# Kernel tuning notes

Measured on AMD Instinct MI355X. Metric: run time of the kernel, lower is better.

## Reference

```python
import jax, jax.numpy as jnp
import numpy as np

B, CI, CO, H, W = 16, 256, 256, 64, 64
WDIM, NUM_FREQ, FREQ_DIM = 512, 16, 512
KS, PAD = 3, 1
SR = 64.0
LR_MULT = 1.0 / SR
GAIN = float(np.sqrt(1.0 / (CI * KS * KS)))
FREQ_GAIN = float(np.sqrt(1.0 / (FREQ_DIM * 2)))


def setup_inputs() -> dict:
    key = jax.random.key(0)
    ks = jax.random.split(key, 7)
    x = jax.random.normal(ks[0], (B, CI, H, W), dtype=jnp.float32)
    temb = jax.random.normal(ks[1], (B, WDIM), dtype=jnp.float32)
    basis = jax.random.normal(ks[2], (CI, KS, KS, FREQ_DIM), dtype=jnp.float32)
    magnitude = jax.random.normal(ks[3], (NUM_FREQ, CI, FREQ_DIM), dtype=jnp.float32)
    out_linear = jax.random.normal(ks[4], (CO, FREQ_DIM), dtype=jnp.float32)
    # FullyConnectedLayer init: weight = randn * (weight_init/lr_mult) = randn (both 1/SR)
    affine_w = jax.random.normal(ks[5], (NUM_FREQ, WDIM), dtype=jnp.float32)
    # bias param stores bias_init / lr_mult = 1 / (1/SR) = SR
    affine_b = jnp.full((NUM_FREQ,), SR, dtype=jnp.float32)
    conv_bias = jnp.zeros((CO,), dtype=jnp.float32)
    return {"x": x, "temb": temb, "basis": basis, "magnitude": magnitude,
            "out_linear": out_linear, "affine_w": affine_w, "affine_b": affine_b,
            "conv_bias": conv_bias}


def reference(x, temb, basis, magnitude, out_linear, affine_w, affine_b, conv_bias):
    # affine (FullyConnectedLayer, linear activation)
    w = affine_w * (LR_MULT / np.sqrt(WDIM))          # weight_gain
    s = temb @ w.T + affine_b * LR_MULT               # [B, K] per-sample freq weights
    # mix magnitude per sample: [K,I,F],[B,K] -> [B,I,F]
    mag_b = jnp.einsum('kif,bk->bif', magnitude, s) / np.sqrt(NUM_FREQ)
    # per-sample dynamic kernels: [I,h,w,F],[B,I,F],[O,F] -> [B,O,I,h,w]
    kernel = jnp.einsum('ihwf,bif,of->boihw', basis, mag_b, out_linear)
    kernel = kernel * (FREQ_GAIN * GAIN)
    kernel = kernel.reshape(B * CO, CI, KS, KS)
    # grouped conv, groups = batch
    xg = x.reshape(1, B * CI, H, W)
    y = jax.lax.conv_general_dilated(
        xg, kernel, window_strides=(1, 1), padding=[(PAD, PAD), (PAD, PAD)],
        dimension_numbers=('NCHW', 'OIHW', 'NCHW'), feature_group_count=B)
    y = y.reshape(B, CO, H, W)
    return jax.nn.silu(y) + conv_bias[None, :, None, None]
```

## Files before the change

kernel.cpp:

```cpp
#include <hip/hip_runtime.h>
#include <hip/hip_bf16.h>
#include <math.h>

#define B_    16
#define CI_   256
#define CO_   256
#define H_    64
#define W_    64
#define WDIM_ 512
#define NF_   16
#define FD_   512

typedef short bf16x8 __attribute__((ext_vector_type(8)));
typedef short s16x8  __attribute__((ext_vector_type(8)));
typedef float f32x4  __attribute__((ext_vector_type(4)));

__device__ __forceinline__ short f2bf(float f) {
  union { float f; unsigned u; } x; x.f = f;
  unsigned r = (x.u + 0x7FFFu + ((x.u >> 16) & 1u)) >> 16;
  return (short)r;
}
__device__ __forceinline__ float bf2f(short s) {
  union { unsigned u; float f; } x; x.u = ((unsigned)(unsigned short)s) << 16;
  return x.f;
}

__device__ __forceinline__ void gload16(const short* g, short* l) {
  __builtin_amdgcn_global_load_lds(
      (const __attribute__((address_space(1))) void*)g,
      (__attribute__((address_space(3))) void*)l, 16, 0, 0);
}

__device__ __forceinline__ size_t koff(int b, int kb, int cc, int t, int o) {
  return ((((((size_t)b * 4 + kb) * 8 + cc) * 9 + t) * 256) + o) * 8;
}
__device__ __forceinline__ size_t xoff(int b, int kb, int cc, int hp, int wp) {
  return ((((((size_t)b * 4 + kb) * 8 + cc) * 66 + hp) * 66) + wp) * 8;
}

__global__ __launch_bounds__(256) void prep_kernel(
    const float* __restrict__ temb, const float* __restrict__ affine_w,
    const float* __restrict__ affine_b, const float* __restrict__ out_linear,
    float* __restrict__ s_ws, short* __restrict__ olbf) {
  int tid = threadIdx.x;
  if (blockIdx.x == 0) {
    int b = tid >> 4, k = tid & 15;
    const float* t = temb + b * WDIM_;
    const float* w = affine_w + k * WDIM_;
    float acc = 0.f;
    for (int j = 0; j < WDIM_; j += 4) {
      float4 tv = *(const float4*)(t + j);
      float4 wv = *(const float4*)(w + j);
      acc += tv.x * wv.x + tv.y * wv.y + tv.z * wv.z + tv.w * wv.w;
    }
    const float WGAIN = 6.9053399e-4f;
    const float LRM   = 1.0f / 64.0f;
    s_ws[tid] = acc * WGAIN + affine_b[k] * LRM;
  } else {
    int e = (blockIdx.x - 1) * 256 + tid;
    const float* src = out_linear + (size_t)e * 8;
    s16x8 pk;
#pragma unroll
    for (int j = 0; j < 8; ++j) pk[j] = f2bf(src[j]);
    *(s16x8*)(olbf + (size_t)e * 8) = pk;
  }
}

__global__ __launch_bounds__(256) void magmix_kernel(
    const float* __restrict__ magnitude, const float* __restrict__ s_ws,
    short* __restrict__ mag_bf) {
  int bid = blockIdx.x;
  int i = bid >> 1;
  int f = ((bid & 1) << 8) + threadIdx.x;
  __shared__ float ssh[256];
  ssh[threadIdx.x] = s_ws[threadIdx.x];
  __syncthreads();
  float mg[16];
#pragma unroll
  for (int k = 0; k < 16; ++k)
    mg[k] = magnitude[(size_t)(k * CI_ + i) * FD_ + f];
#pragma unroll
  for (int b = 0; b < 16; ++b) {
    float acc = 0.f;
#pragma unroll
    for (int k = 0; k < 16; ++k) acc += mg[k] * ssh[b * 16 + k];
    mag_bf[(size_t)(b * CI_ + i) * FD_ + f] = f2bf(acc * 0.25f);
  }
}

__global__ __launch_bounds__(512) void kernsynth_mfma_kernel(
    const float* __restrict__ basis, const short* __restrict__ mag_bf,
    const short* __restrict__ olbf, short* __restrict__ kbf) {
  int bid = blockIdx.x;
  int b  = bid / 18;
  int mt = bid - b * 18;
  int t   = mt >> 1;
  int i0g = (mt & 1) * 128;

  int tid = threadIdx.x;
  int lane = tid & 63;
  int wv = tid >> 6;
  int wm = wv >> 2, wn = wv & 3;
  int l15 = lane & 15, kb = lane >> 4;

  __shared__ short alds[128 * 64];
  __shared__ short blds[256 * 64];

  f32x4 acc[4][4];
#pragma unroll
  for (int m = 0; m < 4; ++m)
#pragma unroll
    for (int n = 0; n < 4; ++n) acc[m][n] = (f32x4)0.f;

  int ra = tid >> 2;
  int fsa = (tid & 3) * 16;
  int rb = tid >> 1;
  int fsb = (tid & 1) * 32;

  const float* bpA = basis + ((size_t)(i0g + ra) * 9 + t) * FD_ + fsa;
  const short* mpA = mag_bf + ((size_t)b * CI_ + i0g + ra) * FD_ + fsa;
  const short* opB = olbf + (size_t)rb * FD_ + fsb;

  for (int cc = 0; cc < 8; ++cc) {
    int f0 = cc * 64;
    __syncthreads();
#pragma unroll
    for (int u = 0; u < 2; ++u) {
      s16x8 m8 = *(const s16x8*)(mpA + f0 + u * 8);
      s16x8 pk;
#pragma unroll
      for (int j = 0; j < 2; ++j) {
        float4 b4 = *(const float4*)(bpA + f0 + u * 8 + j * 4);
        pk[j * 4 + 0] = f2bf(b4.x * bf2f(m8[j * 4 + 0]));
        pk[j * 4 + 1] = f2bf(b4.y * bf2f(m8[j * 4 + 1]));
        pk[j * 4 + 2] = f2bf(b4.z * bf2f(m8[j * 4 + 2]));
        pk[j * 4 + 3] = f2bf(b4.w * bf2f(m8[j * 4 + 3]));
      }
      int slot = (tid & 3) * 2 + u;
      *(s16x8*)&alds[ra * 64 + ((slot ^ (ra & 7)) << 3)] = pk;
    }
#pragma unroll
    for (int u = 0; u < 4; ++u) {
      s16x8 pk = *(const s16x8*)(opB + f0 + u * 8);
      int slot = (tid & 1) * 4 + u;
      *(s16x8*)&blds[rb * 64 + ((slot ^ (rb & 7)) << 3)] = pk;
    }
    __syncthreads();

#pragma unroll
    for (int ks = 0; ks < 2; ++ks) {
      bf16x8 afr[4], bfr[4];
#pragma unroll
      for (int m = 0; m < 4; ++m) {
        int row = wm * 64 + m * 16 + l15;
        int slot = ks * 4 + kb;
        afr[m] = *(const bf16x8*)&alds[row * 64 + ((slot ^ (row & 7)) << 3)];
      }
#pragma unroll
      for (int n = 0; n < 4; ++n) {
        int row = wn * 64 + n * 16 + l15;
        int slot = ks * 4 + kb;
        bfr[n] = *(const bf16x8*)&blds[row * 64 + ((slot ^ (row & 7)) << 3)];
      }
#pragma unroll
      for (int m = 0; m < 4; ++m)
#pragma unroll
        for (int n = 0; n < 4; ++n)
          acc[m][n] = __builtin_amdgcn_mfma_f32_16x16x32_bf16(afr[m], bfr[n], acc[m][n], 0, 0, 0);
    }
  }

  const float KSCALE = 1.0f / 1536.0f;
#pragma unroll
  for (int m = 0; m < 4; ++m) {
    int i_loc = i0g + wm * 64 + m * 16 + (lane >> 4) * 4;
    int kb2 = (i_loc >> 3) & 3;
    int cc2 = i_loc >> 5;
    int e2  = i_loc & 7;
#pragma unroll
    for (int n = 0; n < 4; ++n) {
      int o = wn * 64 + n * 16 + l15;
      short4 s4;
      s4.x = f2bf(acc[m][n][0] * KSCALE);
      s4.y = f2bf(acc[m][n][1] * KSCALE);
      s4.z = f2bf(acc[m][n][2] * KSCALE);
      s4.w = f2bf(acc[m][n][3] * KSCALE);
      *(short4*)(kbf + koff(b, kb2, cc2, t, o) + e2) = s4;
    }
  }
}

__global__ __launch_bounds__(256) void xpose_kernel(
    const float* __restrict__ x, short* __restrict__ xt) {
  int bid = blockIdx.x;
  int b = bid / 66, hp = bid - b * 66;
  int tid = threadIdx.x;
  s16x8 z = (s16x8)0;
  if (hp == 0 || hp == 65) {
    for (int e = tid; e < 32 * 66; e += 256) {
      int s = e / 66, w = e - s * 66;
      *(s16x8*)(xt + xoff(b, s >> 3, s & 7, hp, w)) = z;
    }
    return;
  }
  int h = hp - 1;
  if (tid < 64) {
    int s = tid >> 1, wslot = (tid & 1) ? 65 : 0;
    *(s16x8*)(xt + xoff(b, s >> 3, s & 7, hp, wslot)) = z;
  }
  __shared__ float lx[32 * 64];
  const float* xb = x + ((size_t)b * CI_) * H_ * W_ + (size_t)h * W_;
  int w = tid >> 2, kb = tid & 3;
  for (int cc = 0; cc < 8; ++cc) {
    __syncthreads();
    {
      int rr = tid >> 4, c4 = (tid & 15) * 4;
      float4 v0 = *(const float4*)(xb + (size_t)(cc * 32 + rr) * H_ * W_ + c4);
      *(float4*)&lx[rr * 64 + c4] = v0;
      float4 v1 = *(const float4*)(xb + (size_t)(cc * 32 + rr + 16) * H_ * W_ + c4);
      *(float4*)&lx[(rr + 16) * 64 + c4] = v1;
    }
    __syncthreads();
    s16x8 o8;
#pragma unroll
    for (int k2 = 0; k2 < 8; ++k2) o8[k2] = f2bf(lx[(kb * 8 + k2) * 64 + w]);
    *(s16x8*)(xt + xoff(b, kb, cc, hp, w + 1)) = o8;
  }
}

__global__ __launch_bounds__(256, 4) void conv_mfma_kernel(
    const short* __restrict__ xt, const short* __restrict__ kbf,
    const float* __restrict__ conv_bias, float* __restrict__ out) {
  int bid = ((blockIdx.x & 7) << 7) + (blockIdx.x >> 3);
  int b  = bid >> 6;
  int ot = (bid >> 4) & 3;
  int rt = bid & 15;
  int o_base = ot * 64;
  int r0 = rt * 4;
  int tid = threadIdx.x;
  int lane = tid & 63;
  int wv = tid >> 6;
  int orow = lane & 15, kb = lane >> 4;

  __shared__ short xs[25 * 512];

  f32x4 acc[4][4];
#pragma unroll
  for (int m = 0; m < 4; ++m)
#pragma unroll
    for (int n = 0; n < 4; ++n) acc[m][n] = (f32x4)0.f;

  const short* abase = kbf + koff(b, kb, 0, 0, o_base + orow);

  for (int cc = 0; cc < 8; ++cc) {
    __syncthreads();
    for (int ch = wv; ch < 25; ch += 4) {
      int D = ch * 1024 + lane * 16;
      int kb2 = D / 6400;
      int r = (D - kb2 * 6400) >> 4;
      r = r < 396 ? r : 395;
      int xr = (r * 1986) >> 17;
      int c = r - xr * 66;
      const short* src = xt + xoff(b, kb2, cc, r0 + xr, c);
      gload16(src, &xs[ch * 512]);
    }
    __syncthreads();

    const short* ac = abase + (size_t)cc * 18432;
#pragma unroll
    for (int t = 0; t < 9; ++t) {
      const int dh = t / 3 - 1, dw = t % 3 - 1;
      bf16x8 afr[4], bfr[4];
#pragma unroll
      for (int m = 0; m < 4; ++m)
        afr[m] = *(const bf16x8*)(ac + t * 2048 + m * 128);
      int xr = wv + 1 + dh;
#pragma unroll
      for (int n = 0; n < 4; ++n) {
        int xc = n * 16 + orow + 1 + dw;
        bfr[n] = *(const bf16x8*)&xs[(kb * 400 + xr * 66 + xc) * 8];
      }
#pragma unroll
      for (int m = 0; m < 4; ++m)
#pragma unroll
        for (int n = 0; n < 4; ++n)
          acc[m][n] = __builtin_amdgcn_mfma_f32_16x16x32_bf16(afr[m], bfr[n], acc[m][n], 0, 0, 0);
    }
  }

  int row = r0 + wv;
#pragma unroll
  for (int m = 0; m < 4; ++m) {
#pragma unroll
    for (int q = 0; q < 4; ++q) {
      int o = o_base + m * 16 + (lane >> 4) * 4 + q;
      float bias = conv_bias[o];
      size_t obase = (((size_t)b * CO_ + o) * H_ + row) * W_;
#pragma unroll
      for (int n = 0; n < 4; ++n) {
        float y = acc[m][n][q];
        out[obase + n * 16 + (lane & 15)] = y / (1.f + __expf(-y)) + bias;
      }
    }
  }
}

extern "C" void kernel_launch(void* const* d_in, const int* in_sizes, int n_in,
                              void* d_out, int out_size, void* d_ws, size_t ws_size,
                              hipStream_t stream) {
  const float* x          = (const float*)d_in[0];
  const float* temb       = (const float*)d_in[1];
  const float* basis      = (const float*)d_in[2];
  const float* magnitude  = (const float*)d_in[3];
  const float* out_linear = (const float*)d_in[4];
  const float* affine_w   = (const float*)d_in[5];
  const float* affine_b   = (const float*)d_in[6];
  const float* conv_bias  = (const float*)d_in[7];
  float* out = (float*)d_out;

  char* ws = (char*)d_ws;
  float* s_ws = (float*)ws;
  short* kbf  = (short*)(ws + 1024);
  short* xt   = (short*)(ws + 1024 + 18874368);
  short* mag_bf = (short*)(ws + 1024 + 18874368);
  short* olbf   = (short*)(ws + 1024 + 18874368 + 4194304);

  prep_kernel<<<65, 256, 0, stream>>>(temb, affine_w, affine_b, out_linear, s_ws, olbf);
  magmix_kernel<<<512, 256, 0, stream>>>(magnitude, s_ws, mag_bf);
  kernsynth_mfma_kernel<<<288, 512, 0, stream>>>(basis, mag_bf, olbf, kbf);
  xpose_kernel<<<16 * 66, 256, 0, stream>>>(x, xt);
  conv_mfma_kernel<<<1024, 256, 0, stream>>>(xt, kbf, conv_bias, out);
}
```

Before: 150.1 us.

## Merge kernel synthesis and input transpose into one heterogeneous launch

```diff
diff --git a/kernel.cpp b/kernel.cpp
--- a/kernel.cpp
+++ b/kernel.cpp
@@ -88,143 +88,149 @@
   }
 }
 
-__global__ __launch_bounds__(512) void kernsynth_mfma_kernel(
+__global__ __launch_bounds__(512) void synth_xpose_kernel(
     const float* __restrict__ basis, const short* __restrict__ mag_bf,
-    const short* __restrict__ olbf, short* __restrict__ kbf) {
-  int bid = blockIdx.x;
-  int b  = bid / 18;
-  int mt = bid - b * 18;
-  int t   = mt >> 1;
-  int i0g = (mt & 1) * 128;
-
+    const short* __restrict__ olbf, short* __restrict__ kbf,
+    const float* __restrict__ x, short* __restrict__ xt) {
+  __shared__ short smem_s[24576];
   int tid = threadIdx.x;
-  int lane = tid & 63;
-  int wv = tid >> 6;
-  int wm = wv >> 2, wn = wv & 3;
-  int l15 = lane & 15, kb = lane >> 4;
-
-  __shared__ short alds[128 * 64];
-  __shared__ short blds[256 * 64];
-
-  f32x4 acc[4][4];
-#pragma unroll
-  for (int m = 0; m < 4; ++m)
-#pragma unroll
-    for (int n = 0; n < 4; ++n) acc[m][n] = (f32x4)0.f;
-
-  int ra = tid >> 2;
-  int fsa = (tid & 3) * 16;
-  int rb = tid >> 1;
-  int fsb = (tid & 1) * 32;
-
-  const float* bpA = basis + ((size_t)(i0g + ra) * 9 + t) * FD_ + fsa;
-  const short* mpA = mag_bf + ((size_t)b * CI_ + i0g + ra) * FD_ + fsa;
-  const short* opB = olbf + (size_t)rb * FD_ + fsb;
-
-  for (int cc = 0; cc < 8; ++cc) {
-    int f0 = cc * 64;
-    __syncthreads();
-#pragma unroll
-    for (int u = 0; u < 2; ++u) {
-      s16x8 m8 = *(const s16x8*)(mpA + f0 + u * 8);
-      s16x8 pk;
-#pragma unroll
-      for (int j = 0; j < 2; ++j) {
-        float4 b4 = *(const float4*)(bpA + f0 + u * 8 + j * 4);
-        pk[j * 4 + 0] = f2bf(b4.x * bf2f(m8[j * 4 + 0]));
-        pk[j * 4 + 1] = f2bf(b4.y * bf2f(m8[j * 4 + 1]));
-        pk[j * 4 + 2] = f2bf(b4.z * bf2f(m8[j * 4 + 2]));
-        pk[j * 4 + 3] = f2bf(b4.w * bf2f(m8[j * 4 + 3]));
-      }
-      int slot = (tid & 3) * 2 + u;
-      *(s16x8*)&alds[ra * 64 + ((slot ^ (ra & 7)) << 3)] = pk;
-    }
-#pragma unroll
-    for (int u = 0; u < 4; ++u) {
-      s16x8 pk = *(const s16x8*)(opB + f0 + u * 8);
-      int slot = (tid & 1) * 4 + u;
-      *(s16x8*)&blds[rb * 64 + ((slot ^ (rb & 7)) << 3)] = pk;
-    }
-    __syncthreads();
-
-#pragma unroll
-    for (int ks = 0; ks < 2; ++ks) {
-      bf16x8 afr[4], bfr[4];
-#pragma unroll
-      for (int m = 0; m < 4; ++m) {
-        int row = wm * 64 + m * 16 + l15;
-        int slot = ks * 4 + kb;
-        afr[m] = *(const bf16x8*)&alds[row * 64 + ((slot ^ (row & 7)) << 3)];
-      }
+
+  if (blockIdx.x < 288) {
+    short* alds = smem_s;
+    short* blds = smem_s + 8192;
+    int bid = blockIdx.x;
+    int b  = bid / 18;
+    int mt = bid - b * 18;
+    int t   = mt >> 1;
+    int i0g = (mt & 1) * 128;
+
+    int lane = tid & 63;
+    int wv = tid >> 6;
+    int wm = wv >> 2, wn = wv & 3;
+    int l15 = lane & 15, kb = lane >> 4;
+
+    f32x4 acc[4][4];
+#pragma unroll
+    for (int m = 0; m < 4; ++m)
+#pragma unroll
+      for (int n = 0; n < 4; ++n) acc[m][n] = (f32x4)0.f;
+
+    int ra = tid >> 2;
+    int fsa = (tid & 3) * 16;
+    int rb = tid >> 1;
+    int fsb = (tid & 1) * 32;
+
+    const float* bpA = basis + ((size_t)(i0g + ra) * 9 + t) * FD_ + fsa;
+    const short* mpA = mag_bf + ((size_t)b * CI_ + i0g + ra) * FD_ + fsa;
+    const short* opB = olbf + (size_t)rb * FD_ + fsb;
+
+    for (int cc = 0; cc < 8; ++cc) {
+      int f0 = cc * 64;
+      __syncthreads();
+#pragma unroll
+      for (int u = 0; u < 2; ++u) {
+        s16x8 m8 = *(const s16x8*)(mpA + f0 + u * 8);
+        s16x8 pk;
+#pragma unroll
+        for (int j = 0; j < 2; ++j) {
+          float4 b4 = *(const float4*)(bpA + f0 + u * 8 + j * 4);
+          pk[j * 4 + 0] = f2bf(b4.x * bf2f(m8[j * 4 + 0]));
+          pk[j * 4 + 1] = f2bf(b4.y * bf2f(m8[j * 4 + 1]));
+          pk[j * 4 + 2] = f2bf(b4.z * bf2f(m8[j * 4 + 2]));
+          pk[j * 4 + 3] = f2bf(b4.w * bf2f(m8[j * 4 + 3]));
+        }
+        int slot = (tid & 3) * 2 + u;
+        *(s16x8*)&alds[ra * 64 + ((slot ^ (ra & 7)) << 3)] = pk;
+      }
+#pragma unroll
+      for (int u = 0; u < 4; ++u) {
+        s16x8 pk = *(const s16x8*)(opB + f0 + u * 8);
+        int slot = (tid & 1) * 4 + u;
+        *(s16x8*)&blds[rb * 64 + ((slot ^ (rb & 7)) << 3)] = pk;
+      }
+      __syncthreads();
+
+#pragma unroll
+      for (int ks = 0; ks < 2; ++ks) {
+        bf16x8 afr[4], bfr[4];
+#pragma unroll
+        for (int m = 0; m < 4; ++m) {
+          int row = wm * 64 + m * 16 + l15;
+          int slot = ks * 4 + kb;
+          afr[m] = *(const bf16x8*)&alds[row * 64 + ((slot ^ (row & 7)) << 3)];
+        }
+#pragma unroll
+        for (int n = 0; n < 4; ++n) {
+          int row = wn * 64 + n * 16 + l15;
+          int slot = ks * 4 + kb;
+          bfr[n] = *(const bf16x8*)&blds[row * 64 + ((slot ^ (row & 7)) << 3)];
+        }
+#pragma unroll
+        for (int m = 0; m < 4; ++m)
+#pragma unroll
+          for (int n = 0; n < 4; ++n)
+            acc[m][n] = __builtin_amdgcn_mfma_f32_16x16x32_bf16(afr[m], bfr[n], acc[m][n], 0, 0, 0);
+      }
+    }
+
+    const float KSCALE = 1.0f / 1536.0f;
+#pragma unroll
+    for (int m = 0; m < 4; ++m) {
+      int i_loc = i0g + wm * 64 + m * 16 + (lane >> 4) * 4;
+      int kb2 = (i_loc >> 3) & 3;
+      int cc2 = i_loc >> 5;
+      int e2  = i_loc & 7;
 #pragma unroll
       for (int n = 0; n < 4; ++n) {
-        int row = wn * 64 + n * 16 + l15;
-        int slot = ks * 4 + kb;
-        bfr[n] = *(const bf16x8*)&blds[row * 64 + ((slot ^ (row & 7)) << 3)];
-      }
-#pragma unroll
-      for (int m = 0; m < 4; ++m)
-#pragma unroll
-        for (int n = 0; n < 4; ++n)
-          acc[m][n] = __builtin_amdgcn_mfma_f32_16x16x32_bf16(afr[m], bfr[n], acc[m][n], 0, 0, 0);
-    }
-  }
-
-  const float KSCALE = 1.0f / 1536.0f;
-#pragma unroll
-  for (int m = 0; m < 4; ++m) {
-    int i_loc = i0g + wm * 64 + m * 16 + (lane >> 4) * 4;
-    int kb2 = (i_loc >> 3) & 3;
-    int cc2 = i_loc >> 5;
-    int e2  = i_loc & 7;
-#pragma unroll
-    for (int n = 0; n < 4; ++n) {
-      int o = wn * 64 + n * 16 + l15;
-      short4 s4;
-      s4.x = f2bf(acc[m][n][0] * KSCALE);
-      s4.y = f2bf(acc[m][n][1] * KSCALE);
-      s4.z = f2bf(acc[m][n][2] * KSCALE);
-      s4.w = f2bf(acc[m][n][3] * KSCALE);
-      *(short4*)(kbf + koff(b, kb2, cc2, t, o) + e2) = s4;
-    }
-  }
-}
-
-__global__ __launch_bounds__(256) void xpose_kernel(
-    const float* __restrict__ x, short* __restrict__ xt) {
-  int bid = blockIdx.x;
-  int b = bid / 66, hp = bid - b * 66;
-  int tid = threadIdx.x;
-  s16x8 z = (s16x8)0;
-  if (hp == 0 || hp == 65) {
-    for (int e = tid; e < 32 * 66; e += 256) {
-      int s = e / 66, w = e - s * 66;
-      *(s16x8*)(xt + xoff(b, s >> 3, s & 7, hp, w)) = z;
-    }
-    return;
-  }
-  int h = hp - 1;
-  if (tid < 64) {
-    int s = tid >> 1, wslot = (tid & 1) ? 65 : 0;
-    *(s16x8*)(xt + xoff(b, s >> 3, s & 7, hp, wslot)) = z;
-  }
-  __shared__ float lx[32 * 64];
-  const float* xb = x + ((size_t)b * CI_) * H_ * W_ + (size_t)h * W_;
-  int w = tid >> 2, kb = tid & 3;
-  for (int cc = 0; cc < 8; ++cc) {
-    __syncthreads();
-    {
-      int rr = tid >> 4, c4 = (tid & 15) * 4;
-      float4 v0 = *(const float4*)(xb + (size_t)(cc * 32 + rr) * H_ * W_ + c4);
-      *(float4*)&lx[rr * 64 + c4] = v0;
-      float4 v1 = *(const float4*)(xb + (size_t)(cc * 32 + rr + 16) * H_ * W_ + c4);
-      *(float4*)&lx[(rr + 16) * 64 + c4] = v1;
-    }
-    __syncthreads();
-    s16x8 o8;
-#pragma unroll
-    for (int k2 = 0; k2 < 8; ++k2) o8[k2] = f2bf(lx[(kb * 8 + k2) * 64 + w]);
-    *(s16x8*)(xt + xoff(b, kb, cc, hp, w + 1)) = o8;
+        int o = wn * 64 + n * 16 + l15;
+        short4 s4;
+        s4.x = f2bf(acc[m][n][0] * KSCALE);
+        s4.y = f2bf(acc[m][n][1] * KSCALE);
+        s4.z = f2bf(acc[m][n][2] * KSCALE);
+        s4.w = f2bf(acc[m][n][3] * KSCALE);
+        *(short4*)(kbf + koff(b, kb2, cc2, t, o) + e2) = s4;
+      }
+    }
+  } else {
+    float* lx2 = (float*)smem_s;
+    int bid = blockIdx.x - 288;
+    int b = bid / 33, pr = bid - b * 33;
+    int half = tid >> 8;
+    int t2 = tid & 255;
+    int hp = pr * 2 + half;
+    bool interior = (hp >= 1 && hp <= 64);
+    int h = hp - 1;
+    const float* xb = x + ((size_t)b * CI_) * H_ * W_ + (size_t)h * W_;
+    float* lx = lx2 + half * 2048;
+    s16x8 z = (s16x8)0;
+    int w = t2 >> 2, kb = t2 & 3;
+
+    for (int cc = 0; cc < 8; ++cc) {
+      __syncthreads();
+      if (interior) {
+        int rr = t2 >> 4, c4 = (t2 & 15) * 4;
+        *(float4*)&lx[rr * 64 + c4] =
+            *(const float4*)(xb + (size_t)(cc * 32 + rr) * H_ * W_ + c4);
+        *(float4*)&lx[(rr + 16) * 64 + c4] =
+            *(const float4*)(xb + (size_t)(cc * 32 + rr + 16) * H_ * W_ + c4);
+      }
+      __syncthreads();
+      if (interior) {
+        s16x8 o8;
+#pragma unroll
+        for (int k2 = 0; k2 < 8; ++k2) o8[k2] = f2bf(lx[(kb * 8 + k2) * 64 + w]);
+        *(s16x8*)(xt + xoff(b, kb, cc, hp, w + 1)) = o8;
+        if (w == 0) {
+          *(s16x8*)(xt + xoff(b, kb, cc, hp, 0)) = z;
+          *(s16x8*)(xt + xoff(b, kb, cc, hp, 65)) = z;
+        }
+      } else {
+        for (int e = t2; e < 264; e += 256) {
+          int kb2 = e / 66, wp = e - kb2 * 66;
+          *(s16x8*)(xt + xoff(b, kb2, cc, hp, wp)) = z;
+        }
+      }
+    }
   }
 }
 
@@ -322,12 +328,11 @@
   float* s_ws = (float*)ws;
   short* kbf  = (short*)(ws + 1024);
   short* xt   = (short*)(ws + 1024 + 18874368);
-  short* mag_bf = (short*)(ws + 1024 + 18874368);
-  short* olbf   = (short*)(ws + 1024 + 18874368 + 4194304);
+  short* mag_bf = (short*)(ws + 1024 + 18874368 + 35684352);
+  short* olbf   = (short*)(ws + 1024 + 18874368 + 35684352 + 4194304);
 
   prep_kernel<<<65, 256, 0, stream>>>(temb, affine_w, affine_b, out_linear, s_ws, olbf);
   magmix_kernel<<<512, 256, 0, stream>>>(magnitude, s_ws, mag_bf);
-  kernsynth_mfma_kernel<<<288, 512, 0, stream>>>(basis, mag_bf, olbf, kbf);
-  xpose_kernel<<<16 * 66, 256, 0, stream>>>(x, xt);
+  synth_xpose_kernel<<<816, 512, 0, stream>>>(basis, mag_bf, olbf, kbf, x, xt);
   conv_mfma_kernel<<<1024, 256, 0, stream>>>(xt, kbf, conv_bias, out);
 }
```

After: 136.2 us, median of 2. 1.1x faster.
